# Performance work log

Hardware: AMD Instinct MI355X
Metric: run time of the kernel (lower is better)

The kernel has to match this reference:

```python
import jax, jax.numpy as jnp
import numpy as np

B, N, C = 8, 4096, 1024
ATT_DIM = 512
M = 64  # num_outputs


def setup_inputs() -> dict:
    key = jax.random.key(0)
    k_x, k_w, k_b, k_av = jax.random.split(key, 4)
    x = jax.random.normal(k_x, (B, N, C), dtype=jnp.float32)
    # nn.Linear(input_dim, attention_dim): weight (att, C), bias (att,)
    lim = 1.0 / np.sqrt(C)
    W = jax.random.uniform(k_w, (ATT_DIM, C), dtype=jnp.float32, minval=-lim, maxval=lim)
    b = jax.random.uniform(k_b, (ATT_DIM,), dtype=jnp.float32, minval=-lim, maxval=lim)
    # torch.rand -> uniform [0,1)
    attention_vectors = jax.random.uniform(k_av, (M, ATT_DIM), dtype=jnp.float32)
    return {"x": x, "W": W, "b": b, "attention_vectors": attention_vectors}


def reference(x, W, b, attention_vectors):
    # linear projection: (B,N,C) @ (C,att) + bias -> (B,N,att)
    scores = jnp.einsum('bnc,dc->bnd', x, W) + b
    # learned-query attention logits: (B,M,N)
    logits = jnp.einsum('bnd,md->bmn', scores, attention_vectors)
    weights = jax.nn.softmax(logits, axis=-1)
    # pool original features: (B,M,N) @ (B,N,C) -> (B,M,C)
    return jnp.einsum('bmn,bnc->bmc', weights, x)
```

## Files before the change

kernel.cpp:

```cpp
#include <hip/hip_runtime.h>
#include <hip/hip_bf16.h>

#define Bn 8
#define Nn 4096
#define Cn 1024
#define Dn 512
#define Mn 64

typedef __hip_bfloat16 bf16;
typedef __attribute__((ext_vector_type(8))) short short8;
typedef __attribute__((ext_vector_type(4))) short short4x;
typedef __attribute__((ext_vector_type(4))) float f32x4;

#define MFMA16(a, b, c) __builtin_amdgcn_mfma_f32_16x16x32_bf16((a), (b), (c), 0, 0, 0)

__device__ inline short bfbits(float f) {
  union { bf16 b; short s; } u;
  u.b = __float2bfloat16(f);
  return u.s;
}

__global__ __launch_bounds__(256) void prep_kernel(
    const float* __restrict__ W, const float* __restrict__ bias,
    const float* __restrict__ av, bf16* __restrict__ Vhi,
    bf16* __restrict__ Vlo, float* __restrict__ c0) {
  const int m = blockIdx.x;
  const int t = threadIdx.x;
  const int cl = t & 63, dg = t >> 6;
  const int c = blockIdx.y * 64 + cl;
  const float* wp = W + (size_t)(dg * 128) * Cn + c;
  const float* ap = av + m * Dn + dg * 128;
  float a0 = 0.f, a1 = 0.f, a2 = 0.f, a3 = 0.f;
#pragma unroll 8
  for (int i = 0; i < 128; i += 4) {
    a0 = fmaf(ap[i + 0], wp[(size_t)(i + 0) * Cn], a0);
    a1 = fmaf(ap[i + 1], wp[(size_t)(i + 1) * Cn], a1);
    a2 = fmaf(ap[i + 2], wp[(size_t)(i + 2) * Cn], a2);
    a3 = fmaf(ap[i + 3], wp[(size_t)(i + 3) * Cn], a3);
  }
  __shared__ float red[256];
  red[t] = (a0 + a1) + (a2 + a3);
  __syncthreads();
  const float v = red[cl] + red[cl + 64] + red[cl + 128] + red[cl + 192];
  if (dg == 0) {
    const bf16 hi = __float2bfloat16(v);
    Vhi[m * Cn + c] = hi;
    Vlo[m * Cn + c] = __float2bfloat16(v - __bfloat162float(hi));
  }
  if (blockIdx.y == 0) {
    __syncthreads();
    red[t] = av[m * Dn + t] * bias[t] + av[m * Dn + t + 256] * bias[t + 256];
    __syncthreads();
    if (t < 64) {
      float s = red[t] + red[t + 64] + red[t + 128] + red[t + 192];
#pragma unroll
      for (int off = 32; off > 0; off >>= 1) s += __shfl_down(s, off);
      if (t == 0) c0[m] = s;
    }
  }
}

__global__ __launch_bounds__(256) void logits_kernel(
    const float* __restrict__ x, const bf16* __restrict__ Vhi,
    const bf16* __restrict__ Vlo, const float* __restrict__ c0,
    float* __restrict__ logits) {
  const int n0 = blockIdx.x * 64;
  const int b = blockIdx.y;
  const int t = threadIdx.x;
  const int w = t >> 6, lane = t & 63, lr = lane & 15, q = lane >> 4;
  const float* xrow = x + (size_t)(b * Nn + n0 + w * 16 + lr) * Cn + q * 8;
  f32x4 acc[4];
#pragma unroll
  for (int i = 0; i < 4; ++i) acc[i] = (f32x4){0.f, 0.f, 0.f, 0.f};

  float4 f0 = *(const float4*)(xrow);
  float4 f1 = *(const float4*)(xrow + 4);
  for (int k0 = 0; k0 < Cn; k0 += 32) {
    const float4 c0v = f0, c1v = f1;
    if (k0 + 32 < Cn) {
      f0 = *(const float4*)(xrow + k0 + 32);
      f1 = *(const float4*)(xrow + k0 + 36);
    }
    short8 a;
    a[0] = bfbits(c0v.x); a[1] = bfbits(c0v.y); a[2] = bfbits(c0v.z); a[3] = bfbits(c0v.w);
    a[4] = bfbits(c1v.x); a[5] = bfbits(c1v.y); a[6] = bfbits(c1v.z); a[7] = bfbits(c1v.w);
    const int ka = k0 + q * 8;
#pragma unroll
    for (int mt = 0; mt < 4; ++mt) {
      const short8 bh = *(const short8*)(Vhi + (size_t)(mt * 16 + lr) * Cn + ka);
      acc[mt] = MFMA16(a, bh, acc[mt]);
      const short8 bl = *(const short8*)(Vlo + (size_t)(mt * 16 + lr) * Cn + ka);
      acc[mt] = MFMA16(a, bl, acc[mt]);
    }
  }
#pragma unroll
  for (int mt = 0; mt < 4; ++mt) {
    const int m = mt * 16 + lr;
    const float bb = c0[m];
    float4 o;
    o.x = acc[mt][0] + bb; o.y = acc[mt][1] + bb;
    o.z = acc[mt][2] + bb; o.w = acc[mt][3] + bb;
    *(float4*)&logits[(size_t)(b * Mn + m) * Nn + n0 + w * 16 + q * 4] = o;
  }
}

__global__ __launch_bounds__(256) void softmax_kernel(
    const float* __restrict__ logits, bf16* __restrict__ wgt) {
  const int row = blockIdx.x;
  const int t = threadIdx.x;
  const float* L = logits + (size_t)row * Nn;
  float v[16];
  float mx = -3.4e38f;
#pragma unroll
  for (int i = 0; i < 16; ++i) {
    v[i] = L[t + 256 * i];
    mx = fmaxf(mx, v[i]);
  }
#pragma unroll
  for (int off = 32; off > 0; off >>= 1) mx = fmaxf(mx, __shfl_down(mx, off));
  __shared__ float sred[4];
  if ((t & 63) == 0) sred[t >> 6] = mx;
  __syncthreads();
  mx = fmaxf(fmaxf(sred[0], sred[1]), fmaxf(sred[2], sred[3]));
  float sum = 0.f;
#pragma unroll
  for (int i = 0; i < 16; ++i) {
    v[i] = __expf(v[i] - mx);
    sum += v[i];
  }
#pragma unroll
  for (int off = 32; off > 0; off >>= 1) sum += __shfl_down(sum, off);
  __syncthreads();
  if ((t & 63) == 0) sred[t >> 6] = sum;
  __syncthreads();
  const float inv = 1.f / (sred[0] + sred[1] + sred[2] + sred[3]);
#pragma unroll
  for (int i = 0; i < 16; ++i)
    wgt[(size_t)row * Nn + t + 256 * i] = __float2bfloat16(v[i] * inv);
}

__global__ __launch_bounds__(256) void pool_kernel(
    const float* __restrict__ x, const bf16* __restrict__ wgt,
    float* __restrict__ part) {
  const int cbase = blockIdx.x * 64;
  const int b = blockIdx.y;
  const int ks = blockIdx.z;
  const int t = threadIdx.x;
  __shared__ short XT[64][72];
  const int w = t >> 6, lane = t & 63, lr = lane & 15, q = lane >> 4;
  const int mh = (w & 1) * 32, ch = (w >> 1) * 32;
  f32x4 acc[2][2];
#pragma unroll
  for (int i = 0; i < 2; ++i)
#pragma unroll
    for (int j = 0; j < 2; ++j) acc[i][j] = (f32x4){0.f, 0.f, 0.f, 0.f};

  const int g = t & 15;
  const int h = t >> 4;
  const float* xb = x + (size_t)b * Nn * Cn;
  const bf16* wrow0 = wgt + (size_t)(b * Mn + mh + lr) * Nn;
  const bf16* wrow1 = wgt + (size_t)(b * Mn + mh + 16 + lr) * Nn;

  for (int kc = 0; kc < Nn / 4; kc += 64) {
    const int kglob = ks * (Nn / 4) + kc;
    {
      const float* src = xb + (size_t)(kglob + 4 * g) * Cn + cbase + 4 * h;
      const float4 r0 = *(const float4*)(src);
      const float4 r1 = *(const float4*)(src + Cn);
      const float4 r2 = *(const float4*)(src + 2 * Cn);
      const float4 r3 = *(const float4*)(src + 3 * Cn);
      short4x w0, w1, w2, w3;
      w0[0] = bfbits(r0.x); w0[1] = bfbits(r1.x); w0[2] = bfbits(r2.x); w0[3] = bfbits(r3.x);
      w1[0] = bfbits(r0.y); w1[1] = bfbits(r1.y); w1[2] = bfbits(r2.y); w1[3] = bfbits(r3.y);
      w2[0] = bfbits(r0.z); w2[1] = bfbits(r1.z); w2[2] = bfbits(r2.z); w2[3] = bfbits(r3.z);
      w3[0] = bfbits(r0.w); w3[1] = bfbits(r1.w); w3[2] = bfbits(r2.w); w3[3] = bfbits(r3.w);
      *(short4x*)&XT[4 * h + 0][4 * g] = w0;
      *(short4x*)&XT[4 * h + 1][4 * g] = w1;
      *(short4x*)&XT[4 * h + 2][4 * g] = w2;
      *(short4x*)&XT[4 * h + 3][4 * g] = w3;
    }
    __syncthreads();
#pragma unroll
    for (int kk = 0; kk < 64; kk += 32) {
      const short8 a0 = *(const short8*)(wrow0 + kglob + kk + q * 8);
      const short8 a1 = *(const short8*)(wrow1 + kglob + kk + q * 8);
      const short8 b0 = *(const short8*)&XT[ch + lr][kk + q * 8];
      const short8 b1 = *(const short8*)&XT[ch + 16 + lr][kk + q * 8];
      acc[0][0] = MFMA16(a0, b0, acc[0][0]);
      acc[0][1] = MFMA16(a0, b1, acc[0][1]);
      acc[1][0] = MFMA16(a1, b0, acc[1][0]);
      acc[1][1] = MFMA16(a1, b1, acc[1][1]);
    }
    __syncthreads();
  }
  float* pout = part + ((size_t)ks * Bn + b) * Mn * Cn;
#pragma unroll
  for (int mi = 0; mi < 2; ++mi)
#pragma unroll
    for (int ci = 0; ci < 2; ++ci) {
      const int m = mh + mi * 16 + q * 4;
      const int c = cbase + ch + ci * 16 + lr;
#pragma unroll
      for (int reg = 0; reg < 4; ++reg)
        pout[(size_t)(m + reg) * Cn + c] = acc[mi][ci][reg];
    }
}

__global__ __launch_bounds__(256) void reduce_kernel(
    const float* __restrict__ part, float* __restrict__ out) {
  const int i = blockIdx.x * 256 + threadIdx.x;
  const float4* p = (const float4*)part;
  const int S4 = (Bn * Mn * Cn) / 4;
  const float4 v0 = p[i], v1 = p[i + S4], v2 = p[i + 2 * S4], v3 = p[i + 3 * S4];
  float4 o;
  o.x = (v0.x + v1.x) + (v2.x + v3.x);
  o.y = (v0.y + v1.y) + (v2.y + v3.y);
  o.z = (v0.z + v1.z) + (v2.z + v3.z);
  o.w = (v0.w + v1.w) + (v2.w + v3.w);
  ((float4*)out)[i] = o;
}

extern "C" void kernel_launch(void* const* d_in, const int* in_sizes, int n_in,
                              void* d_out, int out_size, void* d_ws, size_t ws_size,
                              hipStream_t stream) {
  const float* x = (const float*)d_in[0];
  const float* W = (const float*)d_in[1];
  const float* bias = (const float*)d_in[2];
  const float* av = (const float*)d_in[3];
  float* out = (float*)d_out;
  char* ws = (char*)d_ws;

  bf16* Vhi = (bf16*)(ws + 0);
  bf16* Vlo = (bf16*)(ws + 131072);
  float* c0 = (float*)(ws + 262144);
  float* logits = (float*)(ws + 263168);
  bf16* wgt = (bf16*)(ws + 8651776);
  float* part = (float*)(ws + 12846080);

  prep_kernel<<<dim3(Mn, Cn / 64), 256, 0, stream>>>(W, bias, av, Vhi, Vlo, c0);
  logits_kernel<<<dim3(Nn / 64, Bn), 256, 0, stream>>>(x, Vhi, Vlo, c0, logits);
  softmax_kernel<<<Bn * Mn, 256, 0, stream>>>(logits, wgt);
  pool_kernel<<<dim3(Cn / 64, Bn, 4), 256, 0, stream>>>(x, wgt, part);
  reduce_kernel<<<(Bn * Mn * Cn) / 1024, 256, 0, stream>>>(part, out);
}
```

Before: 286.8 us.

## Stage logits and pool operands in LDS with register prefetch and swizzle

The logits kernel now cooperatively loads 64x128 tiles of x (converted to bf16) and the hi/lo V matrices into shared memory. All four waves share the V tiles instead of each wave reading them from global memory, and the next tile is prefetched into registers while MFMAs run. The pool kernel widens its K tile to 128, prefetches the next x tile into registers, and applies an XOR swizzle to the transposed LDS tile to reduce bank conflicts. This costs more LDS per block (about 52KB in logits), which may lower occupancy, and adds extra barriers.

```diff
diff --git a/kernel.cpp b/kernel.cpp
--- a/kernel.cpp
+++ b/kernel.cpp
@@ -67,31 +67,70 @@
   const int n0 = blockIdx.x * 64;
   const int b = blockIdx.y;
   const int t = threadIdx.x;
+  __shared__ short Xs[64][136];
+  __shared__ short VsH[64][136];
+  __shared__ short VsL[64][136];
   const int w = t >> 6, lane = t & 63, lr = lane & 15, q = lane >> 4;
-  const float* xrow = x + (size_t)(b * Nn + n0 + w * 16 + lr) * Cn + q * 8;
+  const ptrdiff_t dlo = Vlo - Vhi;
+
+  int ur[4], uc[4];
+  const float* xsrc[4];
+  const bf16* hsrc[4];
+#pragma unroll
+  for (int j = 0; j < 4; ++j) {
+    const int u = t + 256 * j;
+    ur[j] = u >> 4;
+    uc[j] = (u & 15) * 8;
+    xsrc[j] = x + (size_t)(b * Nn + n0 + ur[j]) * Cn + uc[j];
+    hsrc[j] = Vhi + ur[j] * Cn + uc[j];
+  }
+
   f32x4 acc[4];
 #pragma unroll
   for (int i = 0; i < 4; ++i) acc[i] = (f32x4){0.f, 0.f, 0.f, 0.f};
 
-  float4 f0 = *(const float4*)(xrow);
-  float4 f1 = *(const float4*)(xrow + 4);
-  for (int k0 = 0; k0 < Cn; k0 += 32) {
-    const float4 c0v = f0, c1v = f1;
-    if (k0 + 32 < Cn) {
-      f0 = *(const float4*)(xrow + k0 + 32);
-      f1 = *(const float4*)(xrow + k0 + 36);
-    }
-    short8 a;
-    a[0] = bfbits(c0v.x); a[1] = bfbits(c0v.y); a[2] = bfbits(c0v.z); a[3] = bfbits(c0v.w);
-    a[4] = bfbits(c1v.x); a[5] = bfbits(c1v.y); a[6] = bfbits(c1v.z); a[7] = bfbits(c1v.w);
-    const int ka = k0 + q * 8;
-#pragma unroll
-    for (int mt = 0; mt < 4; ++mt) {
-      const short8 bh = *(const short8*)(Vhi + (size_t)(mt * 16 + lr) * Cn + ka);
-      acc[mt] = MFMA16(a, bh, acc[mt]);
-      const short8 bl = *(const short8*)(Vlo + (size_t)(mt * 16 + lr) * Cn + ka);
-      acc[mt] = MFMA16(a, bl, acc[mt]);
-    }
+  float4 px0[4], px1[4];
+  short8 pvh[4], pvl[4];
+#pragma unroll
+  for (int j = 0; j < 4; ++j) {
+    px0[j] = *(const float4*)(xsrc[j]);
+    px1[j] = *(const float4*)(xsrc[j] + 4);
+    pvh[j] = *(const short8*)(hsrc[j]);
+    pvl[j] = *(const short8*)(hsrc[j] + dlo);
+  }
+
+  for (int k0 = 0; k0 < Cn; k0 += 128) {
+#pragma unroll
+    for (int j = 0; j < 4; ++j) {
+      short8 s;
+      s[0] = bfbits(px0[j].x); s[1] = bfbits(px0[j].y);
+      s[2] = bfbits(px0[j].z); s[3] = bfbits(px0[j].w);
+      s[4] = bfbits(px1[j].x); s[5] = bfbits(px1[j].y);
+      s[6] = bfbits(px1[j].z); s[7] = bfbits(px1[j].w);
+      *(short8*)&Xs[ur[j]][uc[j]] = s;
+      *(short8*)&VsH[ur[j]][uc[j]] = pvh[j];
+      *(short8*)&VsL[ur[j]][uc[j]] = pvl[j];
+    }
+    __syncthreads();
+    if (k0 + 128 < Cn) {
+#pragma unroll
+      for (int j = 0; j < 4; ++j) {
+        px0[j] = *(const float4*)(xsrc[j] + k0 + 128);
+        px1[j] = *(const float4*)(xsrc[j] + k0 + 132);
+        pvh[j] = *(const short8*)(hsrc[j] + k0 + 128);
+        pvl[j] = *(const short8*)(hsrc[j] + dlo + k0 + 128);
+      }
+    }
+#pragma unroll
+    for (int kk = 0; kk < 128; kk += 32) {
+      const short8 a = *(const short8*)&Xs[w * 16 + lr][kk + q * 8];
+#pragma unroll
+      for (int mt = 0; mt < 4; ++mt) {
+        acc[mt] = MFMA16(a, *(const short8*)&VsH[mt * 16 + lr][kk + q * 8], acc[mt]);
+        acc[mt] = MFMA16(a, *(const short8*)&VsL[mt * 16 + lr][kk + q * 8], acc[mt]);
+      }
+    }
+    __syncthreads();
   }
 #pragma unroll
   for (int mt = 0; mt < 4; ++mt) {
@@ -146,7 +185,7 @@
   const int b = blockIdx.y;
   const int ks = blockIdx.z;
   const int t = threadIdx.x;
-  __shared__ short XT[64][72];
+  __shared__ short XT[64][136];
   const int w = t >> 6, lane = t & 63, lr = lane & 15, q = lane >> 4;
   const int mh = (w & 1) * 32, ch = (w >> 1) * 32;
   f32x4 acc[2][2];
@@ -155,37 +194,52 @@
 #pragma unroll
     for (int j = 0; j < 2; ++j) acc[i][j] = (f32x4){0.f, 0.f, 0.f, 0.f};
 
-  const int g = t & 15;
-  const int h = t >> 4;
-  const float* xb = x + (size_t)b * Nn * Cn;
-  const bf16* wrow0 = wgt + (size_t)(b * Mn + mh + lr) * Nn;
-  const bf16* wrow1 = wgt + (size_t)(b * Mn + mh + 16 + lr) * Nn;
-
-  for (int kc = 0; kc < Nn / 4; kc += 64) {
-    const int kglob = ks * (Nn / 4) + kc;
-    {
-      const float* src = xb + (size_t)(kglob + 4 * g) * Cn + cbase + 4 * h;
-      const float4 r0 = *(const float4*)(src);
-      const float4 r1 = *(const float4*)(src + Cn);
-      const float4 r2 = *(const float4*)(src + 2 * Cn);
-      const float4 r3 = *(const float4*)(src + 3 * Cn);
-      short4x w0, w1, w2, w3;
-      w0[0] = bfbits(r0.x); w0[1] = bfbits(r1.x); w0[2] = bfbits(r2.x); w0[3] = bfbits(r3.x);
-      w1[0] = bfbits(r0.y); w1[1] = bfbits(r1.y); w1[2] = bfbits(r2.y); w1[3] = bfbits(r3.y);
-      w2[0] = bfbits(r0.z); w2[1] = bfbits(r1.z); w2[2] = bfbits(r2.z); w2[3] = bfbits(r3.z);
-      w3[0] = bfbits(r0.w); w3[1] = bfbits(r1.w); w3[2] = bfbits(r2.w); w3[3] = bfbits(r3.w);
-      *(short4x*)&XT[4 * h + 0][4 * g] = w0;
-      *(short4x*)&XT[4 * h + 1][4 * g] = w1;
-      *(short4x*)&XT[4 * h + 2][4 * g] = w2;
-      *(short4x*)&XT[4 * h + 3][4 * g] = w3;
-    }
-    __syncthreads();
-#pragma unroll
-    for (int kk = 0; kk < 64; kk += 32) {
-      const short8 a0 = *(const short8*)(wrow0 + kglob + kk + q * 8);
-      const short8 a1 = *(const short8*)(wrow1 + kglob + kk + q * 8);
-      const short8 b0 = *(const short8*)&XT[ch + lr][kk + q * 8];
-      const short8 b1 = *(const short8*)&XT[ch + 16 + lr][kk + q * 8];
+  const int h = t & 15, g = t >> 4;
+  const int swz = 8 * (h & 7);
+  const int swzr0 = 8 * (((ch + lr) >> 2) & 7);
+  const int swzr1 = 8 * (((ch + 16 + lr) >> 2) & 7);
+  const int kbase = ks * (Nn / 4);
+  const float* xsrc = x + (size_t)b * Nn * Cn + (size_t)(kbase + 4 * g) * Cn + cbase + 4 * h;
+  const bf16* wr0 = wgt + (size_t)(b * Mn + mh + lr) * Nn + kbase;
+  const bf16* wr1 = wr0 + (size_t)16 * Nn;
+
+  float4 pf[8];
+#pragma unroll
+  for (int i = 0; i < 4; ++i) {
+    pf[i]     = *(const float4*)(xsrc + (size_t)i * Cn);
+    pf[4 + i] = *(const float4*)(xsrc + (size_t)(64 + i) * Cn);
+  }
+
+  for (int kc = 0; kc < Nn / 4; kc += 128) {
+#pragma unroll
+    for (int blk = 0; blk < 2; ++blk) {
+      const float4 r0 = pf[blk * 4 + 0], r1 = pf[blk * 4 + 1];
+      const float4 r2 = pf[blk * 4 + 2], r3 = pf[blk * 4 + 3];
+      const int kof = (blk * 64 + 4 * g) ^ swz;
+      short4x v0, v1, v2, v3;
+      v0[0] = bfbits(r0.x); v0[1] = bfbits(r1.x); v0[2] = bfbits(r2.x); v0[3] = bfbits(r3.x);
+      v1[0] = bfbits(r0.y); v1[1] = bfbits(r1.y); v1[2] = bfbits(r2.y); v1[3] = bfbits(r3.y);
+      v2[0] = bfbits(r0.z); v2[1] = bfbits(r1.z); v2[2] = bfbits(r2.z); v2[3] = bfbits(r3.z);
+      v3[0] = bfbits(r0.w); v3[1] = bfbits(r1.w); v3[2] = bfbits(r2.w); v3[3] = bfbits(r3.w);
+      *(short4x*)&XT[4 * h + 0][kof] = v0;
+      *(short4x*)&XT[4 * h + 1][kof] = v1;
+      *(short4x*)&XT[4 * h + 2][kof] = v2;
+      *(short4x*)&XT[4 * h + 3][kof] = v3;
+    }
+    __syncthreads();
+    if (kc + 128 < Nn / 4) {
+#pragma unroll
+      for (int i = 0; i < 4; ++i) {
+        pf[i]     = *(const float4*)(xsrc + (size_t)(kc + 128 + i) * Cn);
+        pf[4 + i] = *(const float4*)(xsrc + (size_t)(kc + 192 + i) * Cn);
+      }
+    }
+#pragma unroll
+    for (int kk = 0; kk < 128; kk += 32) {
+      const short8 a0 = *(const short8*)(wr0 + kc + kk + q * 8);
+      const short8 a1 = *(const short8*)(wr1 + kc + kk + q * 8);
+      const short8 b0 = *(const short8*)&XT[ch + lr][(kk + q * 8) ^ swzr0];
+      const short8 b1 = *(const short8*)&XT[ch + 16 + lr][(kk + q * 8) ^ swzr1];
       acc[0][0] = MFMA16(a0, b0, acc[0][0]);
       acc[0][1] = MFMA16(a0, b1, acc[0][1]);
       acc[1][0] = MFMA16(a1, b0, acc[1][0]);
```

Measured after the change: 244.7 us, median of 2. 1.17x faster.
